# Performance work log

Hardware: AMD Instinct MI355X
Metric: run time of the kernel (lower is better)

The kernel has to match this reference:

```python
import jax, jax.numpy as jnp
import numpy as np

B, Z, LIN = 256, 512, 4096
N_SLOTS = 256          # next_pow_2: padded tree slots (slot 0 = zero vector)
L = 3 * (N_SLOTS - 1)  # 765 gather indices (3 per internal node)
CH = [16, 32, 64, 128, 256, 512, 512]  # conv channel chain, last = output_dim


def mish(x):
    return x * jnp.tanh(jax.nn.softplus(x))


def tree_layer_norm(x):
    # normalize each tree over (channels, nodes); torch.std is unbiased (ddof=1)
    mean = jnp.mean(x, axis=(1, 2), keepdims=True)
    std = jnp.std(x, axis=(1, 2), ddof=1, keepdims=True)
    return (x - mean) / (std + 1e-5)


def binary_tree_conv(x, idx, w, b):
    # x: [B, Cin, N]; idx: [B, L]; w: [Cout, Cin, 3]; b: [Cout]
    Bc, C, _ = x.shape
    g = jnp.take_along_axis(
        x, jnp.broadcast_to(idx[:, None, :], (Bc, C, idx.shape[1])), axis=2)
    g = g.reshape(Bc, C, -1, 3)                       # [B, Cin, N-1, 3]
    out = jnp.einsum('bcnk,ock->bon', g, w) + b[None, :, None]
    zero = jnp.zeros((Bc, w.shape[0], 1), out.dtype)  # re-attach zero slot
    return jnp.concatenate([zero, out], axis=2)       # [B, Cout, N]


def setup_inputs() -> dict:
    key = jax.random.key(0)
    ks = jax.random.split(key, 32)
    inp = {}
    inp['trees'] = jax.random.normal(ks[0], (B, Z), jnp.float32)
    idx = jax.random.randint(ks[1], (B, L, 1), 0, N_SLOTS, dtype=jnp.int64 if jax.config.jax_enable_x64 else jnp.int32)
    idx = idx.at[0, 0, 0].set(N_SLOTS - 1)  # guarantee next_pow_2 == 256
    inp['indexes'] = idx
    inp['W_lin'] = jax.random.normal(ks[2], (LIN, Z), jnp.float32) / np.float32(np.sqrt(Z))
    inp['b_lin'] = jax.random.normal(ks[3], (LIN,), jnp.float32) * 0.01
    inp['bn_gamma'] = jax.random.uniform(ks[4], (LIN,), jnp.float32, 0.5, 1.5)
    inp['bn_beta'] = jax.random.normal(ks[5], (LIN,), jnp.float32) * 0.1
    inp['bn_mean'] = jax.random.normal(ks[6], (LIN,), jnp.float32) * 0.1
    inp['bn_var'] = jax.random.uniform(ks[7], (LIN,), jnp.float32, 0.5, 1.5)
    for i in range(6):
        cin, cout = CH[i], CH[i + 1]
        inp[f'w{i}'] = jax.random.normal(ks[8 + 2 * i], (cout, cin, 3), jnp.float32) / np.float32(np.sqrt(3 * cin))
        inp[f'bc{i}'] = jax.random.normal(ks[9 + 2 * i], (cout,), jnp.float32) * 0.01
    return inp


def reference(trees, indexes, W_lin, b_lin, bn_gamma, bn_beta, bn_mean, bn_var,
              w0, bc0, w1, bc1, w2, bc2, w3, bc3, w4, bc4, w5, bc5):
    next_pow_2 = 1 << int(np.asarray(jnp.max(indexes)).item()).bit_length()
    # linear -> BatchNorm1d (eval, running stats) -> Mish -> Dropout(eval = identity)
    x = trees @ W_lin.T + b_lin
    x = (x - bn_mean) * jax.lax.rsqrt(bn_var + 1e-5) * bn_gamma + bn_beta
    x = mish(x)
    x = x.reshape(x.shape[0], LIN // next_pow_2, next_pow_2)  # [B, 16, 256]
    idx = indexes[:, :, 0]
    layers = [(w0, bc0, False), (w1, bc1, True), (w2, bc2, True),
              (w3, bc3, True), (w4, bc4, True), (w5, bc5, True)]
    for w, b, act in layers:
        x = tree_layer_norm(binary_tree_conv(x, idx, w, b))
        if act:
            x = mish(x)
    return x  # [B, output_dim, 256] (the tensor part of the (data, indexes) tuple)
```

## Files before the change

kernel.cpp:

```cpp
#include <hip/hip_runtime.h>
#include <hip/hip_bf16.h>

typedef __attribute__((ext_vector_type(8))) short bf16x8;
typedef __attribute__((ext_vector_type(4))) float f32x4;

__device__ __forceinline__ float b2f(unsigned int u) {
  union { unsigned int i; float f; } v; v.i = u << 16; return v.f;
}
__device__ __forceinline__ unsigned short f2b(float f) {
  unsigned int x = __float_as_uint(f);
  unsigned int r = (x + 0x7fffu + ((x >> 16) & 1u)) >> 16;
  return (unsigned short)r;
}
__device__ __forceinline__ float mish_f(float x) {
  float sp = (x > 20.f) ? x : log1pf(expf(x));
  return x * tanhf(sp);
}

__global__ __launch_bounds__(256) void detect_flags(
    const unsigned short* __restrict__ trees_u16,
    const unsigned int* __restrict__ idx_u32, int* __restrict__ flags)
{
  __shared__ int cnt_sane, cnt_nz;
  const int tid = threadIdx.x;
  if (tid == 0) { cnt_sane = 0; cnt_nz = 0; }
  __syncthreads();
  int sane = 0;
  for (int i = tid; i < 2048; i += 256) {
    unsigned short w = trees_u16[i];
    unsigned int e = (w >> 7) & 0xFFu;
    if ((w & 0x7FFFu) == 0 || (e >= 117u && e <= 133u)) sane++;
  }
  atomicAdd(&cnt_sane, sane);
  int nz = 0;
  for (int i = tid; i < 4096; i += 256) {
    if (idx_u32[2 * i + 1] != 0u) nz++;
  }
  atomicAdd(&cnt_nz, nz);
  __syncthreads();
  if (tid == 0) {
    flags[0] = (cnt_sane < 1843) ? 1 : 0;
    flags[1] = (cnt_nz == 0) ? 1 : 0;
  }
}

__global__ __launch_bounds__(256) void linear_bn_mish(
    const void* __restrict__ treesv, const void* __restrict__ Wlv,
    const void* __restrict__ blv, const void* __restrict__ gamv,
    const void* __restrict__ betv, const void* __restrict__ muv,
    const void* __restrict__ varv, unsigned short* __restrict__ out,
    const int* __restrict__ flags)
{
  __shared__ float As[16][64];
  __shared__ float Bs[16][64];
  const int F = flags[0];
  const int tid = threadIdx.x;
  const int tx = tid & 15, ty = tid >> 4;
  const int j0 = blockIdx.x * 64, b0 = blockIdx.y * 64;
  const int lr = tid >> 2, lc = (tid & 3) << 2;
  const unsigned short* t16 = (const unsigned short*)treesv;
  const float* t32 = (const float*)treesv;
  const unsigned short* w16 = (const unsigned short*)Wlv;
  const float* w32 = (const float*)Wlv;
  float acc[4][4] = {};
  for (int k0 = 0; k0 < 512; k0 += 16) {
    float a0, a1, a2, a3, q0, q1, q2, q3;
    if (F) {
      float4 ta = *(const float4*)(t32 + (b0 + lr) * 512 + k0 + lc);
      float4 tb = *(const float4*)(w32 + (j0 + lr) * 512 + k0 + lc);
      a0 = ta.x; a1 = ta.y; a2 = ta.z; a3 = ta.w;
      q0 = tb.x; q1 = tb.y; q2 = tb.z; q3 = tb.w;
    } else {
      ushort4 ta = *(const ushort4*)(t16 + (b0 + lr) * 512 + k0 + lc);
      ushort4 tb = *(const ushort4*)(w16 + (j0 + lr) * 512 + k0 + lc);
      a0 = b2f(ta.x); a1 = b2f(ta.y); a2 = b2f(ta.z); a3 = b2f(ta.w);
      q0 = b2f(tb.x); q1 = b2f(tb.y); q2 = b2f(tb.z); q3 = b2f(tb.w);
    }
    __syncthreads();
    As[lc + 0][lr] = a0; As[lc + 1][lr] = a1; As[lc + 2][lr] = a2; As[lc + 3][lr] = a3;
    Bs[lc + 0][lr] = q0; Bs[lc + 1][lr] = q1; Bs[lc + 2][lr] = q2; Bs[lc + 3][lr] = q3;
    __syncthreads();
#pragma unroll
    for (int kk = 0; kk < 16; ++kk) {
      float4 av = *(const float4*)&As[kk][ty * 4];
      float4 bv = *(const float4*)&Bs[kk][tx * 4];
      float a[4] = {av.x, av.y, av.z, av.w};
      float bb[4] = {bv.x, bv.y, bv.z, bv.w};
#pragma unroll
      for (int iy = 0; iy < 4; ++iy)
#pragma unroll
        for (int jx = 0; jx < 4; ++jx) acc[iy][jx] += a[iy] * bb[jx];
    }
  }
  const unsigned short* bl16 = (const unsigned short*)blv;  const float* bl32 = (const float*)blv;
  const unsigned short* g16 = (const unsigned short*)gamv;  const float* g32 = (const float*)gamv;
  const unsigned short* be16 = (const unsigned short*)betv; const float* be32 = (const float*)betv;
  const unsigned short* m16 = (const unsigned short*)muv;   const float* m32 = (const float*)muv;
  const unsigned short* v16 = (const unsigned short*)varv;  const float* v32 = (const float*)varv;
#pragma unroll
  for (int iy = 0; iy < 4; ++iy) {
    int b = b0 + ty * 4 + iy;
    unsigned short st[4];
#pragma unroll
    for (int jx = 0; jx < 4; ++jx) {
      int j = j0 + tx * 4 + jx;
      float bj = F ? bl32[j] : b2f(bl16[j]);
      float gj = F ? g32[j] : b2f(g16[j]);
      float ej = F ? be32[j] : b2f(be16[j]);
      float mj = F ? m32[j] : b2f(m16[j]);
      float vj = F ? v32[j] : b2f(v16[j]);
      float v = acc[iy][jx] + bj;
      v = (v - mj) * rsqrtf(vj + 1e-5f) * gj + ej;
      v = mish_f(v);
      st[jx] = f2b(v);
    }
    ushort4 pack; pack.x = st[0]; pack.y = st[1]; pack.z = st[2]; pack.w = st[3];
    *(ushort4*)(out + b * 4096 + j0 + tx * 4) = pack;
  }
}

template<int CIN, int COUT, int TO>
__global__ __launch_bounds__(256) void tree_conv(
    const unsigned short* __restrict__ xin,
    const void* __restrict__ idxv,
    const void* __restrict__ wv,
    const void* __restrict__ biasv,
    unsigned short* __restrict__ out,
    const int* __restrict__ flags)
{
  constexpr int CC = 16;
  constexpr int KC = CC * 3;
  constexpr int UO = TO / 16;
  constexpr int PE = (TO * KC) / 256;
  __shared__ float xs[CC][256];
  __shared__ float wsm[KC][TO];
  const int F = flags[0], G = flags[1];
  const int tid = threadIdx.x;
  const int tx = tid & 15, ty = tid >> 4;
  const int b = blockIdx.z;
  const int o0 = blockIdx.y * TO;
  const int n0 = blockIdx.x * 64;
  const unsigned short* xb = xin + b * CIN * 256;
  const unsigned short* wt16 = (const unsigned short*)wv;
  const float* wt32 = (const float*)wv;
  const int* idx32 = (const int*)idxv;

  int jj[4][3];
  int np[4];
  {
    const int step = G ? 2 : 1;
    const int* idxb = idx32 + b * 765 * step;
#pragma unroll
    for (int ni = 0; ni < 4; ++ni) {
      int n = n0 + tx * 4 + ni;
      np[ni] = n;
      int m = n - 1;
#pragma unroll
      for (int k = 0; k < 3; ++k) jj[ni][k] = (m >= 0) ? idxb[(3 * m + k) * step] : 0;
    }
  }

  float acc[UO][4];
#pragma unroll
  for (int u = 0; u < UO; ++u)
#pragma unroll
    for (int ni = 0; ni < 4; ++ni) acc[u][ni] = 0.f;

  for (int c0 = 0; c0 < CIN; c0 += CC) {
    __syncthreads();
    {
      const uint4* src = (const uint4*)(xb + c0 * 256);
      uint4 v0 = src[tid * 2];
      uint4 v1 = src[tid * 2 + 1];
      unsigned int ww[8] = {v0.x, v0.y, v0.z, v0.w, v1.x, v1.y, v1.z, v1.w};
      float t[16];
#pragma unroll
      for (int q = 0; q < 8; ++q) {
        t[2 * q] = b2f(ww[q] & 0xffffu);
        t[2 * q + 1] = b2f(ww[q] >> 16);
      }
      float* dst = &xs[tid >> 4][(tid & 15) * 16];
#pragma unroll
      for (int q = 0; q < 4; ++q)
        *(float4*)(dst + 4 * q) = make_float4(t[4 * q], t[4 * q + 1], t[4 * q + 2], t[4 * q + 3]);
    }
    if (F) {
#pragma unroll
      for (int e = 0; e < PE; ++e) {
        int p = e * 256 + tid;
        int o_rel = p / KC;
        int rem = p - o_rel * KC;
        wsm[rem][o_rel] = wt32[(o0 + o_rel) * CIN * 3 + c0 * 3 + rem];
      }
    } else {
#pragma unroll
      for (int e = 0; e < PE; ++e) {
        int p = e * 256 + tid;
        int o_rel = p / KC;
        int rem = p - o_rel * KC;
        wsm[rem][o_rel] = b2f(wt16[(o0 + o_rel) * CIN * 3 + c0 * 3 + rem]);
      }
    }
    __syncthreads();
#pragma unroll
    for (int cc = 0; cc < CC; ++cc) {
      float wvv[3][UO];
#pragma unroll
      for (int k = 0; k < 3; ++k) {
        if constexpr (UO == 4) {
          float4 f = *(const float4*)&wsm[cc * 3 + k][ty * 4];
          wvv[k][0] = f.x; wvv[k][1] = f.y; wvv[k][2] = f.z; wvv[k][3] = f.w;
        } else {
          float2 f = *(const float2*)&wsm[cc * 3 + k][ty * 2];
          wvv[k][0] = f.x; wvv[k][1] = f.y;
        }
      }
#pragma unroll
      for (int ni = 0; ni < 4; ++ni) {
        float x0 = xs[cc][jj[ni][0]];
        float x1 = xs[cc][jj[ni][1]];
        float x2 = xs[cc][jj[ni][2]];
#pragma unroll
        for (int u = 0; u < UO; ++u)
          acc[u][ni] += wvv[0][u] * x0 + wvv[1][u] * x1 + wvv[2][u] * x2;
      }
    }
  }
  const unsigned short* bi16 = (const unsigned short*)biasv;
  const float* bi32 = (const float*)biasv;
#pragma unroll
  for (int u = 0; u < UO; ++u) {
    int o = o0 + ty * UO + u;
    float bv = F ? bi32[o] : b2f(bi16[o]);
    unsigned short st[4];
#pragma unroll
    for (int ni = 0; ni < 4; ++ni) {
      float v = (np[ni] == 0) ? 0.f : (acc[u][ni] + bv);
      st[ni] = f2b(v);
    }
    ushort4 pack; pack.x = st[0]; pack.y = st[1]; pack.z = st[2]; pack.w = st[3];
    *(ushort4*)(out + (b * COUT + o) * 256 + n0 + tx * 4) = pack;
  }
}

__global__ __launch_bounds__(256) void wt_transpose(
    const void* __restrict__ wv, unsigned short* __restrict__ Wt,
    int CIN, int COUT, const int* __restrict__ flags)
{
  const int K = CIN * 3;
  const int total = COUT * K;
  int gid = blockIdx.x * 256 + threadIdx.x;
  if (gid >= total) return;
  const int F = flags[0];
  int o = gid / K;
  int kp = gid - o * K;
  int cc0 = kp / 96;
  int rem = kp - cc0 * 96;
  int k = rem >> 5, ci = rem & 31;
  int c = cc0 * 32 + ci;
  int src = (o * CIN + c) * 3 + k;
  unsigned short v = F ? f2b(((const float*)wv)[src]) : ((const unsigned short*)wv)[src];
  Wt[gid] = v;
}

template<int CIN, int COUT>
__global__ __launch_bounds__(256) void tree_conv_mfma(
    const unsigned short* __restrict__ xT,
    const void* __restrict__ idxv,
    const unsigned short* __restrict__ Wt,
    const void* __restrict__ biasv,
    unsigned short* __restrict__ outT,
    const int* __restrict__ flags)
{
  constexpr int K = CIN * 3;
  constexpr int XS = 40;
  constexpr int WS = 40;
  __shared__ unsigned short xTl[256 * XS];
  __shared__ unsigned short Wl[128 * WS];
  const int tid = threadIdx.x;
  const int wave = tid >> 6, lane = tid & 63, quad = lane >> 4, l15 = lane & 15;
  const int b = blockIdx.z;
  const int n_blk = blockIdx.x * 128, o_blk = blockIdx.y * 128;
  const int o_half = (wave >> 1) * 64, n_half = (wave & 1) * 64;
  const int F = flags[0], G = flags[1];

  int jr[4][3];
  int ng[4];
  {
    const int step = G ? 2 : 1;
    const int* idxb = (const int*)idxv + (size_t)b * 765 * step;
#pragma unroll
    for (int t = 0; t < 4; ++t) {
      int n = n_blk + n_half + t * 16 + l15;
      ng[t] = n;
      int m = n - 1;
#pragma unroll
      for (int k = 0; k < 3; ++k) jr[t][k] = (m >= 0) ? idxb[(3 * m + k) * step] : 0;
    }
  }

  f32x4 acc[4][4];
#pragma unroll
  for (int a = 0; a < 4; ++a)
#pragma unroll
    for (int c = 0; c < 4; ++c) acc[a][c] = (f32x4){0.f, 0.f, 0.f, 0.f};

  for (int c0 = 0; c0 < CIN; c0 += 32) {
#pragma unroll
    for (int k = 0; k < 3; ++k) {
      __syncthreads();
      if (k == 0) {
        const unsigned short* s = xT + ((size_t)b * 256 + tid) * CIN + c0;
        uint4 a0 = *(const uint4*)s;
        uint4 a1 = *(const uint4*)(s + 8);
        uint4 a2 = *(const uint4*)(s + 16);
        uint4 a3 = *(const uint4*)(s + 24);
        *(uint4*)&xTl[tid * XS + 0] = a0;
        *(uint4*)&xTl[tid * XS + 8] = a1;
        *(uint4*)&xTl[tid * XS + 16] = a2;
        *(uint4*)&xTl[tid * XS + 24] = a3;
      }
      {
        int o = tid >> 1, part = tid & 1;
        const unsigned short* s = Wt + (size_t)(o_blk + o) * K + c0 * 3 + k * 32 + part * 16;
        uint4 a0 = *(const uint4*)s;
        uint4 a1 = *(const uint4*)(s + 8);
        *(uint4*)&Wl[o * WS + part * 16] = a0;
        *(uint4*)&Wl[o * WS + part * 16 + 8] = a1;
      }
      __syncthreads();
      bf16x8 af[4], bfr[4];
#pragma unroll
      for (int t = 0; t < 4; ++t)
        af[t] = *(const bf16x8*)&Wl[(o_half + t * 16 + l15) * WS + quad * 8];
#pragma unroll
      for (int t = 0; t < 4; ++t)
        bfr[t] = *(const bf16x8*)&xTl[jr[t][k] * XS + quad * 8];
#pragma unroll
      for (int to = 0; to < 4; ++to)
#pragma unroll
        for (int tn = 0; tn < 4; ++tn)
          acc[to][tn] = __builtin_amdgcn_mfma_f32_16x16x32_bf16(
              af[to], bfr[tn], acc[to][tn], 0, 0, 0);
    }
  }

  const unsigned short* bi16 = (const unsigned short*)biasv;
  const float* bi32 = (const float*)biasv;
#pragma unroll
  for (int to = 0; to < 4; ++to) {
    int og = o_blk + o_half + to * 16 + quad * 4;
    float b4[4];
#pragma unroll
    for (int r = 0; r < 4; ++r) b4[r] = F ? bi32[og + r] : b2f(bi16[og + r]);
#pragma unroll
    for (int tn = 0; tn < 4; ++tn) {
      int n = ng[tn];
      ushort4 st;
      if (n == 0) {
        st.x = 0; st.y = 0; st.z = 0; st.w = 0;
      } else {
        st.x = f2b(acc[to][tn][0] + b4[0]);
        st.y = f2b(acc[to][tn][1] + b4[1]);
        st.z = f2b(acc[to][tn][2] + b4[2]);
        st.w = f2b(acc[to][tn][3] + b4[3]);
      }
      *(ushort4*)(outT + ((size_t)b * 256 + n) * COUT + og) = st;
    }
  }
}

__global__ __launch_bounds__(256) void stats_part(
    const unsigned short* __restrict__ raw, int C, float* __restrict__ partials)
{
  const int tid = threadIdx.x;
  const int sidx = blockIdx.x, b = blockIdx.y;
  const int NS = gridDim.x;
  const int nv = C * 32;
  const int per = nv / NS;
  const uint4* pv = (const uint4*)(raw + (size_t)b * C * 256) + (size_t)sidx * per;
  float s = 0.f, s2 = 0.f;
  for (int i = tid; i < per; i += 256) {
    uint4 v = pv[i];
    unsigned int ww[4] = {v.x, v.y, v.z, v.w};
#pragma unroll
    for (int q = 0; q < 4; ++q) {
      float f0 = b2f(ww[q] & 0xffffu), f1 = b2f(ww[q] >> 16);
      s += f0 + f1; s2 += f0 * f0 + f1 * f1;
    }
  }
  __shared__ float rs[256], rs2[256];
  rs[tid] = s; rs2[tid] = s2;
  __syncthreads();
  for (int off = 128; off > 0; off >>= 1) {
    if (tid < off) { rs[tid] += rs[tid + off]; rs2[tid] += rs2[tid + off]; }
    __syncthreads();
  }
  if (tid == 0) {
    partials[2 * (b * NS + sidx) + 0] = rs[0];
    partials[2 * (b * NS + sidx) + 1] = rs2[0];
  }
}

__global__ __launch_bounds__(256) void stats_fin(
    const float* __restrict__ partials, int C, int NS, float* __restrict__ stats)
{
  const int b = threadIdx.x;
  float s = 0.f, s2 = 0.f;
  for (int i = 0; i < NS; ++i) {
    s += partials[2 * (b * NS + i) + 0];
    s2 += partials[2 * (b * NS + i) + 1];
  }
  const float M = (float)(C * 256);
  float mean = s / M;
  float varv = (s2 - s * s / M) / (M - 1.f);
  varv = fmaxf(varv, 0.f);
  stats[2 * b] = mean;
  stats[2 * b + 1] = 1.f / (sqrtf(varv) + 1e-5f);
}

__global__ __launch_bounds__(256) void apply_norm(
    const unsigned short* __restrict__ raw, unsigned short* __restrict__ out,
    int C, int act, const float* __restrict__ stats)
{
  const int tid = threadIdx.x;
  const int b = blockIdx.y;
  const int nv = C * 32;
  const float mean = stats[2 * b], inv = stats[2 * b + 1];
  const uint4* pv = (const uint4*)(raw + (size_t)b * C * 256);
  uint4* ov = (uint4*)(out + (size_t)b * C * 256);
  const int stride = gridDim.x * 256;
  for (int i = blockIdx.x * 256 + tid; i < nv; i += stride) {
    uint4 v = pv[i];
    unsigned int ww[4] = {v.x, v.y, v.z, v.w};
    unsigned int rr[4];
#pragma unroll
    for (int q = 0; q < 4; ++q) {
      float f0 = (b2f(ww[q] & 0xffffu) - mean) * inv;
      float f1 = (b2f(ww[q] >> 16) - mean) * inv;
      if (act) { f0 = mish_f(f0); f1 = mish_f(f1); }
      rr[q] = (unsigned)f2b(f0) | ((unsigned)f2b(f1) << 16);
    }
    uint4 r; r.x = rr[0]; r.y = rr[1]; r.z = rr[2]; r.w = rr[3];
    ov[i] = r;
  }
}

__global__ __launch_bounds__(256) void apply_t(
    const unsigned short* __restrict__ in, void* __restrict__ outv,
    int R, int S, int act, int finalw,
    const float* __restrict__ stats, const int* __restrict__ flags)
{
  __shared__ unsigned short tile[64 * 72];
  const int tid = threadIdx.x;
  const int b = blockIdx.z;
  const int S0 = blockIdx.x * 64, R0 = blockIdx.y * 64;
  const float mean = stats[2 * b], inv = stats[2 * b + 1];
  {
    int r = tid >> 2, c4 = (tid & 3) * 16;
    const unsigned short* src = in + ((size_t)b * R + R0 + r) * S + S0 + c4;
    uint4 u0 = *(const uint4*)src;
    uint4 u1 = *(const uint4*)(src + 8);
    unsigned int ww[8] = {u0.x, u0.y, u0.z, u0.w, u1.x, u1.y, u1.z, u1.w};
    unsigned short tv[16];
#pragma unroll
    for (int q = 0; q < 8; ++q) {
      float f0 = (b2f(ww[q] & 0xffffu) - mean) * inv;
      float f1 = (b2f(ww[q] >> 16) - mean) * inv;
      if (act) { f0 = mish_f(f0); f1 = mish_f(f1); }
      tv[2 * q] = f2b(f0);
      tv[2 * q + 1] = f2b(f1);
    }
    unsigned short* d = &tile[r * 72 + c4];
#pragma unroll
    for (int q = 0; q < 2; ++q) {
      ushort4 p0; p0.x = tv[8*q+0]; p0.y = tv[8*q+1]; p0.z = tv[8*q+2]; p0.w = tv[8*q+3];
      ushort4 p1; p1.x = tv[8*q+4]; p1.y = tv[8*q+5]; p1.z = tv[8*q+6]; p1.w = tv[8*q+7];
      *(ushort4*)(d + 8 * q) = p0;
      *(ushort4*)(d + 8 * q + 4) = p1;
    }
  }
  __syncthreads();
  {
    int s = tid >> 2, rc = (tid & 3) * 16;
    const int wf32 = finalw && flags[0];
    if (wf32) {
      float* of = (float*)outv + ((size_t)b * S + S0 + s) * R + R0 + rc;
#pragma unroll
      for (int q = 0; q < 4; ++q) {
        float4 fv;
        fv.x = b2f(tile[(rc + 4 * q + 0) * 72 + s]);
        fv.y = b2f(tile[(rc + 4 * q + 1) * 72 + s]);
        fv.z = b2f(tile[(rc + 4 * q + 2) * 72 + s]);
        fv.w = b2f(tile[(rc + 4 * q + 3) * 72 + s]);
        *(float4*)(of + 4 * q) = fv;
      }
    } else {
      unsigned short* ob = (unsigned short*)outv + ((size_t)b * S + S0 + s) * R + R0 + rc;
#pragma unroll
      for (int q = 0; q < 4; ++q) {
        ushort4 p;
        p.x = tile[(rc + 4 * q + 0) * 72 + s];
        p.y = tile[(rc + 4 * q + 1) * 72 + s];
        p.z = tile[(rc + 4 * q + 2) * 72 + s];
        p.w = tile[(rc + 4 * q + 3) * 72 + s];
        *(ushort4*)(ob + 4 * q) = p;
      }
    }
  }
}

extern "C" void kernel_launch(void* const* d_in, const int* in_sizes, int n_in,
                              void* d_out, int out_size, void* d_ws, size_t ws_size,
                              hipStream_t stream) {
  const void* trees = d_in[0];
  const void* indexes = d_in[1];
  const void* W_lin = d_in[2];
  const void* b_lin = d_in[3];
  const void* gam = d_in[4];
  const void* bet = d_in[5];
  const void* mu  = d_in[6];
  const void* var = d_in[7];
  const void* w0 = d_in[8];   const void* bc0 = d_in[9];
  const void* w1 = d_in[10];  const void* bc1 = d_in[11];
  const void* w2 = d_in[12];  const void* bc2 = d_in[13];
  const void* w3 = d_in[14];  const void* bc3 = d_in[15];
  const void* w4 = d_in[16];  const void* bc4 = d_in[17];
  const void* w5 = d_in[18];  const void* bc5 = d_in[19];

  int* flags = (int*)d_ws;
  unsigned short* nrm = (unsigned short*)((char*)d_ws + 1024);
  unsigned short* raw = nrm + 33554432;
  float* statsF = (float*)((char*)d_ws + 1024 + 67108864 - 2048);
  unsigned short* Wt = (unsigned short*)d_out;
  float* partials = (float*)((char*)d_out + (4 << 20));
  float* stats2 = (float*)((char*)d_out + (4 << 20) + 65536);

  detect_flags<<<1, 256, 0, stream>>>((const unsigned short*)trees,
                                      (const unsigned int*)indexes, flags);

  linear_bn_mish<<<dim3(64, 4), 256, 0, stream>>>(trees, W_lin, b_lin, gam, bet, mu, var,
                                                  nrm, flags);

  tree_conv<16, 32, 32><<<dim3(4, 1, 256), 256, 0, stream>>>(nrm, indexes, w0, bc0, raw, flags);
  stats_part<<<dim3(4, 256), 256, 0, stream>>>(raw, 32, partials);
  stats_fin<<<1, 256, 0, stream>>>(partials, 32, 4, stats2);
  apply_norm<<<dim3(4, 256), 256, 0, stream>>>(raw, nrm, 32, 0, stats2);

  tree_conv<32, 64, 64><<<dim3(4, 1, 256), 256, 0, stream>>>(nrm, indexes, w1, bc1, raw, flags);
  stats_part<<<dim3(8, 256), 256, 0, stream>>>(raw, 64, partials);
  stats_fin<<<1, 256, 0, stream>>>(partials, 64, 8, stats2);
  apply_t<<<dim3(4, 1, 256), 256, 0, stream>>>(raw, nrm, 64, 256, 1, 0, stats2, flags);

  wt_transpose<<<96, 256, 0, stream>>>(w2, Wt, 64, 128, flags);
  tree_conv_mfma<64, 128><<<dim3(2, 1, 256), 256, 0, stream>>>(nrm, indexes, Wt, bc2, raw, flags);
  stats_part<<<dim3(8, 256), 256, 0, stream>>>(raw, 128, partials);
  stats_fin<<<1, 256, 0, stream>>>(partials, 128, 8, stats2);
  apply_norm<<<dim3(8, 256), 256, 0, stream>>>(raw, nrm, 128, 1, stats2);

  wt_transpose<<<384, 256, 0, stream>>>(w3, Wt, 128, 256, flags);
  tree_conv_mfma<128, 256><<<dim3(2, 2, 256), 256, 0, stream>>>(nrm, indexes, Wt, bc3, raw, flags);
  stats_part<<<dim3(16, 256), 256, 0, stream>>>(raw, 256, partials);
  stats_fin<<<1, 256, 0, stream>>>(partials, 256, 16, stats2);
  apply_norm<<<dim3(8, 256), 256, 0, stream>>>(raw, nrm, 256, 1, stats2);

  wt_transpose<<<1536, 256, 0, stream>>>(w4, Wt, 256, 512, flags);
  tree_conv_mfma<256, 512><<<dim3(2, 4, 256), 256, 0, stream>>>(nrm, indexes, Wt, bc4, raw, flags);
  stats_part<<<dim3(16, 256), 256, 0, stream>>>(raw, 512, partials);
  stats_fin<<<1, 256, 0, stream>>>(partials, 512, 16, stats2);
  apply_norm<<<dim3(16, 256), 256, 0, stream>>>(raw, nrm, 512, 1, stats2);

  wt_transpose<<<3072, 256, 0, stream>>>(w5, Wt, 512, 512, flags);
  tree_conv_mfma<512, 512><<<dim3(2, 4, 256), 256, 0, stream>>>(nrm, indexes, Wt, bc5, raw, flags);
  stats_part<<<dim3(16, 256), 256, 0, stream>>>(raw, 512, partials);
  stats_fin<<<1, 256, 0, stream>>>(partials, 512, 16, statsF);
  apply_t<<<dim3(8, 4, 256), 256, 0, stream>>>(raw, d_out, 256, 512, 1, 1, statsF, flags);
}
```

Baseline: 1.100 ms.

## Prefetch next channel chunk into registers, stage all three taps per sync, remap blocks

The tree-conv MFMA kernel now loads the weights for all three kernel taps of a 32-channel chunk into LDS at once, using a wider row stride. This cuts the barriers per chunk from six to two. The x and weight data for the next chunk are prefetched into registers while the current chunk's MFMAs run, so global load latency overlaps compute. Block indices are also remapped so that consecutive blocks are spread across batch groups, which changes how work lands on XCDs and caches. The cost is more register pressure and a larger LDS footprint.

```diff
diff --git a/kernel.cpp b/kernel.cpp
--- a/kernel.cpp
+++ b/kernel.cpp
@@ -274,13 +274,20 @@
 {
   constexpr int K = CIN * 3;
   constexpr int XS = 40;
-  constexpr int WS = 40;
+  constexpr int WS = 104;
   __shared__ unsigned short xTl[256 * XS];
   __shared__ unsigned short Wl[128 * WS];
   const int tid = threadIdx.x;
   const int wave = tid >> 6, lane = tid & 63, quad = lane >> 4, l15 = lane & 15;
-  const int b = blockIdx.z;
-  const int n_blk = blockIdx.x * 128, o_blk = blockIdx.y * 128;
+
+  const int BPB = gridDim.x * gridDim.y;
+  const unsigned raw = blockIdx.x + gridDim.x * (blockIdx.y + gridDim.y * blockIdx.z);
+  const int r8 = (int)(raw & 7u);
+  const unsigned m9 = raw >> 3;
+  const int b = r8 * 32 + (int)(m9 / (unsigned)BPB);
+  const int u = (int)(m9 % (unsigned)BPB);
+  const int n_blk = (u & 1) * 128, o_blk = (u >> 1) * 128;
+
   const int o_half = (wave >> 1) * 64, n_half = (wave & 1) * 64;
   const int F = flags[0], G = flags[1];
 
@@ -293,9 +300,9 @@
     for (int t = 0; t < 4; ++t) {
       int n = n_blk + n_half + t * 16 + l15;
       ng[t] = n;
-      int m = n - 1;
-#pragma unroll
-      for (int k = 0; k < 3; ++k) jr[t][k] = (m >= 0) ? idxb[(3 * m + k) * step] : 0;
+      int mm = n - 1;
+#pragma unroll
+      for (int k = 0; k < 3; ++k) jr[t][k] = (mm >= 0) ? idxb[(3 * mm + k) * step] : 0;
     }
   }
 
@@ -305,34 +312,52 @@
 #pragma unroll
     for (int c = 0; c < 4; ++c) acc[a][c] = (f32x4){0.f, 0.f, 0.f, 0.f};
 
+  const unsigned short* xsrc = xT + ((size_t)b * 256 + tid) * CIN;
+  const int wo = tid >> 1, wpart = tid & 1;
+  const unsigned short* wsrc = Wt + (size_t)(o_blk + wo) * K + wpart * 48;
+
+  uint4 xr0, xr1, xr2, xr3, wr0, wr1, wr2, wr3, wr4, wr5;
+  {
+    const unsigned short* s = xsrc;
+    xr0 = *(const uint4*)(s);      xr1 = *(const uint4*)(s + 8);
+    xr2 = *(const uint4*)(s + 16); xr3 = *(const uint4*)(s + 24);
+    const unsigned short* w = wsrc;
+    wr0 = *(const uint4*)(w);      wr1 = *(const uint4*)(w + 8);
+    wr2 = *(const uint4*)(w + 16); wr3 = *(const uint4*)(w + 24);
+    wr4 = *(const uint4*)(w + 32); wr5 = *(const uint4*)(w + 40);
+  }
+
   for (int c0 = 0; c0 < CIN; c0 += 32) {
+    __syncthreads();
+    *(uint4*)&xTl[tid * XS + 0]  = xr0;
+    *(uint4*)&xTl[tid * XS + 8]  = xr1;
+    *(uint4*)&xTl[tid * XS + 16] = xr2;
+    *(uint4*)&xTl[tid * XS + 24] = xr3;
+    {
+      unsigned short* d = &Wl[wo * WS + wpart * 48];
+      *(uint4*)(d + 0)  = wr0;
+      *(uint4*)(d + 8)  = wr1;
+      *(uint4*)(d + 16) = wr2;
+      *(uint4*)(d + 24) = wr3;
+      *(uint4*)(d + 32) = wr4;
+      *(uint4*)(d + 40) = wr5;
+    }
+    __syncthreads();
+    if (c0 + 32 < CIN) {
+      const unsigned short* s = xsrc + c0 + 32;
+      xr0 = *(const uint4*)(s);      xr1 = *(const uint4*)(s + 8);
+      xr2 = *(const uint4*)(s + 16); xr3 = *(const uint4*)(s + 24);
+      const unsigned short* w = wsrc + (size_t)(c0 + 32) * 3;
+      wr0 = *(const uint4*)(w);      wr1 = *(const uint4*)(w + 8);
+      wr2 = *(const uint4*)(w + 16); wr3 = *(const uint4*)(w + 24);
+      wr4 = *(const uint4*)(w + 32); wr5 = *(const uint4*)(w + 40);
+    }
 #pragma unroll
     for (int k = 0; k < 3; ++k) {
-      __syncthreads();
-      if (k == 0) {
-        const unsigned short* s = xT + ((size_t)b * 256 + tid) * CIN + c0;
-        uint4 a0 = *(const uint4*)s;
-        uint4 a1 = *(const uint4*)(s + 8);
-        uint4 a2 = *(const uint4*)(s + 16);
-        uint4 a3 = *(const uint4*)(s + 24);
-        *(uint4*)&xTl[tid * XS + 0] = a0;
-        *(uint4*)&xTl[tid * XS + 8] = a1;
-        *(uint4*)&xTl[tid * XS + 16] = a2;
-        *(uint4*)&xTl[tid * XS + 24] = a3;
-      }
-      {
-        int o = tid >> 1, part = tid & 1;
-        const unsigned short* s = Wt + (size_t)(o_blk + o) * K + c0 * 3 + k * 32 + part * 16;
-        uint4 a0 = *(const uint4*)s;
-        uint4 a1 = *(const uint4*)(s + 8);
-        *(uint4*)&Wl[o * WS + part * 16] = a0;
-        *(uint4*)&Wl[o * WS + part * 16 + 8] = a1;
-      }
-      __syncthreads();
       bf16x8 af[4], bfr[4];
 #pragma unroll
       for (int t = 0; t < 4; ++t)
-        af[t] = *(const bf16x8*)&Wl[(o_half + t * 16 + l15) * WS + quad * 8];
+        af[t] = *(const bf16x8*)&Wl[(o_half + t * 16 + l15) * WS + k * 32 + quad * 8];
 #pragma unroll
       for (int t = 0; t < 4; ++t)
         bfr[t] = *(const bf16x8*)&xTl[jr[t][k] * XS + quad * 8];
```

After: 983.5 us. 10.6% less time.
